# Performance work log

Measured on AMD Instinct MI355X. Metric: run time of the kernel, lower is better.

The kernel has to match this reference:

```python
import jax, jax.numpy as jnp
import numpy as np

N, B, T, D = 6, 4, 1024, 768
P = 3            # number of prior phases
H, Dh = 2, 32    # n_heads, head_dim
I = H * Dh       # inner_dim
EPS = 1e-5


def setup_inputs() -> dict:
    key = jax.random.key(0)
    ks = jax.random.split(key, 9)
    current_states = jax.random.normal(ks[0], (N, B, T, D), dtype=jnp.float32)
    history_states = jax.random.normal(ks[1], (P, N, B, T, D), dtype=jnp.float32)
    attention_mask = jax.random.randint(ks[2], (B, T), 0, 2, dtype=jnp.int32)
    # Linear weights stored as [in, out] (transposed nn.Linear weight)
    s = 1.0 / np.sqrt(D)
    Wq = jax.random.uniform(ks[3], (N, D, I), jnp.float32, -s, s)  # per-domain q proj
    Wk = jax.random.uniform(ks[4], (D, I), jnp.float32, -s, s)     # shared k proj
    Wv = jax.random.uniform(ks[5], (D, I), jnp.float32, -s, s)     # shared v proj
    so = 1.0 / np.sqrt(I)
    Wo = jax.random.uniform(ks[6], (N, I, D), jnp.float32, -so, so)  # per-domain out proj
    gamma = jnp.ones((N, D), jnp.float32)   # per-domain LayerNorm weight
    beta = jnp.zeros((N, D), jnp.float32)   # per-domain LayerNorm bias
    return {"current_states": current_states, "history_states": history_states,
            "attention_mask": attention_mask, "Wq": Wq, "Wk": Wk, "Wv": Wv,
            "Wo": Wo, "gamma": gamma, "beta": beta}


def reference(current_states, history_states, attention_mask, Wq, Wk, Wv, Wo, gamma, beta):
    x = current_states                                   # [N,B,T,D]
    # concat prior phases along time per domain: [N,B,P*T,D]
    prior = jnp.transpose(history_states, (1, 2, 0, 3, 4)).reshape(N, B, P * T, D)

    q = jnp.einsum('nbtd,ndi->nbti', x, Wq).reshape(N, B, T, H, Dh).transpose(0, 1, 3, 2, 4)       # [N,B,H,T,Dh]
    k = jnp.einsum('nbsd,di->nbsi', prior, Wk).reshape(N, B, P * T, H, Dh).transpose(0, 1, 3, 2, 4)  # [N,B,H,S,Dh]
    v = jnp.einsum('nbsd,di->nbsi', prior, Wv).reshape(N, B, P * T, H, Dh).transpose(0, 1, 3, 2, 4)

    scale = 1.0 / jnp.sqrt(jnp.float32(Dh))
    scores = jnp.einsum('nbhtd,nbhsd->nbhts', q, k) * scale  # [N,B,H,T,P*T]
    full_mask = jnp.tile(attention_mask.astype(jnp.float32), (1, P))  # [B,P*T]
    bias = (1.0 - full_mask)[None, :, None, None, :] * -10000.0
    attn = jax.nn.softmax(scores + bias, axis=-1)
    o = jnp.einsum('nbhts,nbhsd->nbhtd', attn, v)            # [N,B,H,T,Dh]
    o = o.transpose(0, 1, 3, 2, 4).reshape(N, B, T, I)       # [N,B,T,I]
    o = jnp.einsum('nbti,nid->nbtd', o, Wo)                  # [N,B,T,D]

    y = x + o  # residual (dropout p=0)
    mu = jnp.mean(y, axis=-1, keepdims=True)
    var = jnp.mean(jnp.square(y - mu), axis=-1, keepdims=True)
    out = (y - mu) * jax.lax.rsqrt(var + EPS)
    out = out * gamma[:, None, None, :] + beta[:, None, None, :]
    return out
```

## Files before the change

### kernel.cpp

```cpp
#include <hip/hip_runtime.h>
#include <hip/hip_bf16.h>
#include <math.h>

#define NDOM 6
#define BB 4
#define TT 1024
#define DD 768
#define PP 3
#define HH 2
#define DHH 32
#define II 64
#define SS (PP*TT)
#define NROW (NDOM*BB*TT)
#define NKVROW (NDOM*BB*SS)
#define NSPLIT 8
#define NITER (SS/NSPLIT/64)
#define NKVB (NKVROW/128)
#define NQB  (NROW/128)
#define LNEPS 1e-5f

typedef unsigned int uint;
typedef uint  u32x4  __attribute__((ext_vector_type(4)));
typedef int   i32x2  __attribute__((ext_vector_type(2)));
typedef float f32x2  __attribute__((ext_vector_type(2)));
typedef float f32x4  __attribute__((ext_vector_type(4)));
typedef float f32x16 __attribute__((ext_vector_type(16)));
typedef __bf16 bf16x8 __attribute__((ext_vector_type(8)));

__device__ __forceinline__ f32x16 mfma32(u32x4 a, u32x4 b, f32x16 c) {
  return __builtin_amdgcn_mfma_f32_32x32x16_bf16(
      __builtin_bit_cast(bf16x8, a), __builtin_bit_cast(bf16x8, b), c, 0, 0, 0);
}

__device__ __forceinline__ uint pkbf(float a, float b) {
  union { __bf16 h[2]; uint u; } v;
  v.h[0] = (__bf16)a; v.h[1] = (__bf16)b;
  return v.u;
}
__device__ __forceinline__ float b2f(uint u16) {
  union { uint i; float f; } v; v.i = u16 << 16; return v.f;
}

__device__ __forceinline__ void plswap(uint a, uint b, uint& x, uint& y) {
#if __has_builtin(__builtin_amdgcn_permlane32_swap)
  i32x2 r = __builtin_amdgcn_permlane32_swap((int)a, (int)b, false, false);
  x = (uint)r.x; y = (uint)r.y;
#else
  uint sa = __shfl_xor(a, 32), sb = __shfl_xor(b, 32);
  bool h1 = (threadIdx.x & 32) != 0;
  x = h1 ? sb : a;
  y = h1 ? b : sa;
#endif
}

#if __has_builtin(__builtin_amdgcn_global_load_lds)
#define HAS_GLL 1
typedef __attribute__((address_space(3))) uint lds_u32;
typedef __attribute__((address_space(1))) uint glb_u32;
__device__ __forceinline__ void gll16(const void* src, void* lds_base) {
  __builtin_amdgcn_global_load_lds((const glb_u32*)src, (lds_u32*)lds_base, 16, 0, 0);
}
#else
#define HAS_GLL 0
#endif

__global__ __launch_bounds__(256) void prep_kernel(
    const int* __restrict__ mask, const float* __restrict__ Wk,
    const float* __restrict__ Wv, const float* __restrict__ Wq,
    const float* __restrict__ Wo,
    __hip_bfloat16* __restrict__ Bkv, __hip_bfloat16* __restrict__ Bq,
    __hip_bfloat16* __restrict__ Bo, float* __restrict__ bias2)
{
  int i = blockIdx.x * 256 + threadIdx.x;
  const int N1 = 128 * 768;
  const int N2 = NDOM * 64 * 768;
  const int N3 = NDOM * 768 * 64;
  if (i < N1) {
    int c = i / 768, kd = i % 768;
    int e = kd & 7, ud = (kd >> 3) & 7, kk = kd >> 6;
    int k = (kk << 6) + ((ud ^ (c & 7)) << 3) + e;
    float v = (c < 64) ? Wk[k * 64 + c] : Wv[k * 64 + (c - 64)];
    Bkv[i] = __float2bfloat16(v);
  } else if (i < N1 + N2) {
    int j = i - N1;
    int n = j / (64 * 768);
    int rem = j % (64 * 768);
    int c = rem / 768, kd = rem % 768;
    int e = kd & 7, ud = (kd >> 3) & 7, kk = kd >> 6;
    int k = (kk << 6) + ((ud ^ (c & 7)) << 3) + e;
    Bq[j] = __float2bfloat16(Wq[((size_t)n * 768 + k) * 64 + c]);
  } else if (i < N1 + N2 + N3) {
    int j = i - N1 - N2;
    int n = j / (768 * 64);
    int rem = j % (768 * 64);
    int d = rem / 64, k = rem % 64;
    Bo[j] = __float2bfloat16(Wo[((size_t)n * 64 + k) * 768 + d]);
  } else if (i < N1 + N2 + N3 + BB * SS) {
    int j = i - N1 - N2 - N3;
    int b = j / SS, s = j % SS;
    bias2[j] = (1.0f - (float)mask[b * TT + (s & (TT - 1))]) * (-14426.950408889634f);
  }
}

__global__ __launch_bounds__(256) void qkv_gemm_kernel(
    const float* __restrict__ x, const float* __restrict__ hist,
    const __hip_bfloat16* __restrict__ Bkv, const __hip_bfloat16* __restrict__ Bq,
    __hip_bfloat16* __restrict__ Qo, __hip_bfloat16* __restrict__ Kh,
    __hip_bfloat16* __restrict__ Vt2)
{
  __shared__ float As[128 * 64];
  __shared__ __hip_bfloat16 Bs[128 * 64];
  const int tid = threadIdx.x;
  const int lane = tid & 63, w = tid >> 6;
  const int cl = lane & 31, hi = lane >> 5;

  const bool isKV = blockIdx.x < NKVB;
  const float* Asrc;
  int nb = 0, s0 = 0, n = 0, brow = 0;
  if (isKV) {
    brow = blockIdx.x * 128;
    nb = brow / SS; n = nb >> 2;
    int b = nb & 3;
    s0 = brow % SS;
    int p = s0 / TT, t0 = s0 % TT;
    Asrc = hist + (((size_t)(p * NDOM + n) * BB + b) * TT + t0) * 768;
  } else {
    brow = (blockIdx.x - NKVB) * 128;
    n = brow >> 12;
    Asrc = x + (size_t)brow * 768;
  }
  const __hip_bfloat16* Bsrc = isKV ? Bkv : (Bq + (size_t)n * 64 * 768);
  const int BROWS = isKV ? 128 : 64;
  const int NACC = isKV ? 4 : 2;

  f32x16 acc[4] = {};

  const int lrow16 = lane >> 4, lslot16 = lane & 15;
  const int lrow8  = lane >> 3, lslot8  = lane & 7;

  for (int kk = 0; kk < 12; ++kk) {
#pragma unroll
    for (int j = 0; j < 8; ++j) {
      int row0 = w * 32 + j * 4;
      int row = row0 + lrow16;
      int gs = lslot16 ^ (row & 15);
      const float* src = Asrc + (size_t)row * 768 + kk * 64 + gs * 4;
#if HAS_GLL
      gll16(src, &As[row0 * 64]);
#else
      *(f32x4*)(&As[row0 * 64] + lane * 4) = *(const f32x4*)src;
#endif
    }
    {
      int perw = BROWS / 4;
#pragma unroll
      for (int j = 0; j < 4; ++j) {
        if (j * 8 < perw) {
          int c0 = w * perw + j * 8;
          int c = c0 + lrow8;
          const __hip_bfloat16* src = Bsrc + (size_t)c * 768 + kk * 64 + lslot8 * 8;
#if HAS_GLL
          gll16(src, &Bs[c0 * 64]);
#else
          *(u32x4*)(&Bs[c0 * 64] + lane * 8) = *(const u32x4*)src;
#endif
        }
      }
    }
    __syncthreads();

    {
      const int row = w * 32 + cl;
#pragma unroll
      for (int ks = 0; ks < 4; ++ks) {
        int t = ks * 4 + hi * 2;
        f32x4 a0 = *(const f32x4*)&As[row * 64 + ((t       ^ (row & 15)) * 4)];
        f32x4 a1 = *(const f32x4*)&As[row * 64 + (((t + 1) ^ (row & 15)) * 4)];
        u32x4 a = {pkbf(a0.x, a0.y), pkbf(a0.z, a0.w), pkbf(a1.x, a1.y), pkbf(a1.z, a1.w)};
        int u0 = ks * 2 + hi;
#pragma unroll
        for (int g = 0; g < 4; ++g) {
          if (g < NACC) {
            int c = g * 32 + cl;
            u32x4 b = *(const u32x4*)&Bs[c * 64 + ((u0 ^ (c & 7)) * 8)];
            acc[g] = mfma32(a, b, acc[g]);
          }
        }
      }
    }
    __syncthreads();
  }

  if (isKV) {
    {
      const size_t base0 = (size_t)(nb * 2 + 0) * SS;
      const size_t base1 = (size_t)(nb * 2 + 1) * SS;
#pragma unroll
      for (int r = 0; r < 16; ++r) {
        int rl = (r & 3) + 8 * (r >> 2) + 4 * hi;
        int s  = s0 + w * 32 + rl;
        Kh[(base0 + s) * 32 + cl] = __float2bfloat16(acc[0][r]);
        Kh[(base1 + s) * 32 + cl] = __float2bfloat16(acc[1][r]);
      }
    }
#pragma unroll
    for (int k = 0; k < 4; ++k) {
      int sb = (s0 + w * 32 + 8 * k) >> 3;
      size_t A0 = (((size_t)(nb * 2 + 0) * (SS / 8) + sb) * 32 + cl) * 8 + 4 * hi;
      size_t A1 = (((size_t)(nb * 2 + 1) * (SS / 8) + sb) * 32 + cl) * 8 + 4 * hi;
      *(uint2*)(Vt2 + A0) = uint2{pkbf(acc[2][4*k], acc[2][4*k+1]), pkbf(acc[2][4*k+2], acc[2][4*k+3])};
      *(uint2*)(Vt2 + A1) = uint2{pkbf(acc[3][4*k], acc[3][4*k+1]), pkbf(acc[3][4*k+2], acc[3][4*k+3])};
    }
  } else {
#pragma unroll
    for (int r = 0; r < 16; ++r) {
      int rl = (r & 3) + 8 * (r >> 2) + 4 * hi;
      size_t rb = (size_t)(brow + w * 32 + rl) * 64;
      Qo[rb + cl]      = __float2bfloat16(acc[0][r]);
      Qo[rb + 32 + cl] = __float2bfloat16(acc[1][r]);
    }
  }
}

struct KV { u32x4 k0, k1, k2, k3, v0, v1, v2, v3; };

__global__ __launch_bounds__(256) void attn_kernel(
    const __hip_bfloat16* __restrict__ Q, const __hip_bfloat16* __restrict__ Kh,
    const __hip_bfloat16* __restrict__ Vt2, const float* __restrict__ bias2,
    __hip_bfloat16* __restrict__ Op, float* __restrict__ Mp, float* __restrict__ Lp)
{
  const int tid = threadIdx.x;
  const int lane = tid & 63, w = tid >> 6;
  const int cl = lane & 31, hi = lane >> 5;
  const int bid = blockIdx.x;
  const int g = bid % 48;
  const int rest = bid / 48;
  const int sp = rest >> 3;
  const int tq = rest & 7;
  const int qtile = tq * 4 + w;
  const int h = g & 1, nb = g >> 1;
  const int b = nb & 3;
  const int qrow = nb * TT + qtile * 32;
  const int sbase = sp * (SS / NSPLIT);

  const __hip_bfloat16* Qp = Q + (size_t)(qrow + cl) * 64 + h * 32 + hi * 8;
  u32x4 qf0 = *(const u32x4*)Qp;
  u32x4 qf1 = *(const u32x4*)(Qp + 16);

  const __hip_bfloat16* Kp = Kh + ((size_t)(nb * 2 + h) * SS + sbase) * 32;
  const __hip_bfloat16* Vp = Vt2 + (size_t)(nb * 2 + h) * SS * 32 + (size_t)sbase * 32;
  const float* Bp = bias2 + b * SS + sbase + hi * 4;

  const float scale2 = 0.17677669529663687f * 1.4426950408889634f;
  const f32x2 sc2 = {scale2, scale2};

  f32x16 ot = {};
  float m = -1e30f, lsum = 0.f;

  auto loadKV = [&](int it) {
    KV t;
    const __hip_bfloat16* kp = Kp + (size_t)it * 64 * 32;
    t.k0 = *(const u32x4*)(kp + cl * 32 + hi * 8);
    t.k1 = *(const u32x4*)(kp + cl * 32 + 16 + hi * 8);
    t.k2 = *(const u32x4*)(kp + 1024 + cl * 32 + hi * 8);
    t.k3 = *(const u32x4*)(kp + 1024 + cl * 32 + 16 + hi * 8);
    const __hip_bfloat16* vp = Vp + (size_t)it * 64 * 32;
    t.v0 = *(const u32x4*)(vp + ((0 * 2 + hi) * 32 + cl) * 8);
    t.v1 = *(const u32x4*)(vp + ((1 * 2 + hi) * 32 + cl) * 8);
    t.v2 = *(const u32x4*)(vp + ((2 * 2 + hi) * 32 + cl) * 8);
    t.v3 = *(const u32x4*)(vp + ((3 * 2 + hi) * 32 + cl) * 8);
    return t;
  };

  auto compute = [&](const KV& t, int it) {
    f32x16 pz0 = {}, pz1 = {};
    pz0 = mfma32(t.k0, qf0, pz0);
    pz0 = mfma32(t.k1, qf1, pz0);
    pz1 = mfma32(t.k2, qf0, pz1);
    pz1 = mfma32(t.k3, qf1, pz1);
    const float* bp = Bp + it * 64;
    f32x4 b4[8];
#pragma unroll
    for (int q = 0; q < 8; ++q) b4[q] = *(const f32x4*)(bp + 8 * q);
    f32x2 p2[16];
#pragma unroll
    for (int i = 0; i < 8; ++i) {
      f32x4 bq0 = b4[i >> 1];
      f32x4 bq1 = b4[4 + (i >> 1)];
      f32x2 bv0 = (i & 1) ? f32x2{bq0.z, bq0.w} : f32x2{bq0.x, bq0.y};
      f32x2 bv1 = (i & 1) ? f32x2{bq1.z, bq1.w} : f32x2{bq1.x, bq1.y};
      p2[i]     = f32x2{pz0[2*i], pz0[2*i+1]} * sc2 + bv0;
      p2[8 + i] = f32x2{pz1[2*i], pz1[2*i+1]} * sc2 + bv1;
    }
    f32x2 mx = p2[0];
#pragma unroll
    for (int i = 1; i < 16; ++i) {
      mx.x = fmaxf(mx.x, p2[i].x);
      mx.y = fmaxf(mx.y, p2[i].y);
    }
    float tm = fmaxf(mx.x, mx.y);
    tm = fmaxf(tm, __shfl_xor(tm, 32));
    if (!__all(tm - m <= 8.f)) {
      float mn = fmaxf(m, tm);
      float f = exp2f(m - mn);
#pragma unroll
      for (int i = 0; i < 16; ++i) ot[i] *= f;
      lsum *= f;
      m = mn;
    }
    const f32x2 m2 = {m, m};
    f32x2 s2 = {0.f, 0.f};
#pragma unroll
    for (int i = 0; i < 16; ++i) {
      f32x2 d = p2[i] - m2;
      f32x2 e = {exp2f(d.x), exp2f(d.y)};
      p2[i] = e;
      s2 += e;
    }
    float ts = s2.x + s2.y;
    ts += __shfl_xor(ts, 32);
    lsum += ts;
    uint cv[16];
#pragma unroll
    for (int i = 0; i < 16; ++i) cv[i] = pkbf(p2[i].x, p2[i].y);
    u32x4 pf0, pf1, pf2, pf3;
    {
      uint x0, y0, x1, y1;
      plswap(cv[0], cv[2],  x0, y0); plswap(cv[1], cv[3],  x1, y1);
      pf0 = u32x4{x0, x1, y0, y1};
      plswap(cv[4], cv[6],  x0, y0); plswap(cv[5], cv[7],  x1, y1);
      pf1 = u32x4{x0, x1, y0, y1};
      plswap(cv[8], cv[10], x0, y0); plswap(cv[9], cv[11], x1, y1);
      pf2 = u32x4{x0, x1, y0, y1};
      plswap(cv[12], cv[14], x0, y0); plswap(cv[13], cv[15], x1, y1);
      pf3 = u32x4{x0, x1, y0, y1};
    }
    ot = mfma32(t.v0, pf0, ot);
    ot = mfma32(t.v1, pf1, ot);
    ot = mfma32(t.v2, pf2, ot);
    ot = mfma32(t.v3, pf3, ot);
  };

  KV cur = loadKV(0);
#pragma unroll 1
  for (int it = 0; it < NITER; ++it) {
    KV nxt = loadKV(it + 1 < NITER ? it + 1 : NITER - 1);
    compute(cur, it);
    cur = nxt;
    __builtin_amdgcn_s_barrier();
  }

  __hip_bfloat16* op = Op + ((size_t)sp * NROW + qrow + cl) * 64 + h * 32 + 4 * hi;
#pragma unroll
  for (int k = 0; k < 4; ++k) {
    uint2 wv = {pkbf(ot[4*k], ot[4*k+1]), pkbf(ot[4*k+2], ot[4*k+3])};
    *(uint2*)(op + 8 * k) = wv;
  }
  if (lane < 32) {
    int mi = ((sp * 24 + nb) * 2 + h) * TT + qtile * 32 + cl;
    Mp[mi] = m;
    Lp[mi] = lsum;
  }
}

__global__ __launch_bounds__(256) void oproj_ln_kernel(
    const float* __restrict__ x, const __hip_bfloat16* __restrict__ Op,
    const float* __restrict__ Mp, const float* __restrict__ Lp,
    const __hip_bfloat16* __restrict__ Bo, const float* __restrict__ gamma,
    const float* __restrict__ beta, float* __restrict__ out)
{
  __shared__ float red[4][32][2];
  __shared__ float redf[32][2];
  const int tid = threadIdx.x;
  const int lane = tid & 63, w = tid >> 6;
  const int cl = lane & 31, hi = lane >> 5;
  const int row0 = blockIdx.x * 32;
  const int n = row0 >> 12;
  const int nb = row0 >> 10;
  const int trow = (row0 & 1023) + cl;
  const int MLS = 24 * 2 * TT;

  float wsp[2][NSPLIT];
#pragma unroll
  for (int h = 0; h < 2; ++h) {
    int mi = (nb * 2 + h) * TT + trow;
    float mv[NSPLIT], lv[NSPLIT];
#pragma unroll
    for (int sp = 0; sp < NSPLIT; ++sp) { mv[sp] = Mp[mi + sp * MLS]; lv[sp] = Lp[mi + sp * MLS]; }
    float ms = mv[0];
#pragma unroll
    for (int sp = 1; sp < NSPLIT; ++sp) ms = fmaxf(ms, mv[sp]);
    float den = 0.f;
#pragma unroll
    for (int sp = 0; sp < NSPLIT; ++sp) { wsp[h][sp] = exp2f(mv[sp] - ms); den = fmaf(lv[sp], wsp[h][sp], den); }
    float inv = 1.0f / den;
#pragma unroll
    for (int sp = 0; sp < NSPLIT; ++sp) wsp[h][sp] *= inv;
  }

  u32x4 af[4];
#pragma unroll
  for (int ks = 0; ks < 4; ++ks) {
    int h = ks >> 1;
    size_t off = (size_t)(row0 + cl) * 64 + ks * 16 + hi * 8;
    f32x2 s0 = {}, s1 = {}, s2 = {}, s3 = {};
#pragma unroll
    for (int sp = 0; sp < NSPLIT; ++sp) {
      u32x4 v = *(const u32x4*)(Op + (size_t)sp * NROW * 64 + off);
      float wv = wsp[h][sp];
      s0 += f32x2{b2f(v[0] & 0xffffu), b2f(v[0] >> 16)} * wv;
      s1 += f32x2{b2f(v[1] & 0xffffu), b2f(v[1] >> 16)} * wv;
      s2 += f32x2{b2f(v[2] & 0xffffu), b2f(v[2] >> 16)} * wv;
      s3 += f32x2{b2f(v[3] & 0xffffu), b2f(v[3] >> 16)} * wv;
    }
    af[ks] = u32x4{pkbf(s0.x, s0.y), pkbf(s1.x, s1.y), pkbf(s2.x, s2.y), pkbf(s3.x, s3.y)};
  }

  const __hip_bfloat16* Bp = Bo + ((size_t)n * 768 + w * 192 + cl) * 64 + hi * 8;
  f32x16 acc[6] = {};
#pragma unroll
  for (int ks = 0; ks < 4; ++ks) {
#pragma unroll
    for (int t = 0; t < 6; ++t) {
      u32x4 bb = *(const u32x4*)(Bp + (size_t)(t * 32) * 64 + ks * 16);
      acc[t] = mfma32(af[ks], bb, acc[t]);
    }
  }

  float s1[16], s2[16];
#pragma unroll
  for (int r = 0; r < 16; ++r) { s1[r] = 0.f; s2[r] = 0.f; }
#pragma unroll
  for (int t = 0; t < 6; ++t) {
#pragma unroll
    for (int r = 0; r < 16; ++r) {
      int R = (r & 3) + 8 * (r >> 2) + 4 * hi;
      int col = w * 192 + t * 32 + cl;
      float y = acc[t][r] + x[(size_t)(row0 + R) * 768 + col];
      acc[t][r] = y;
      s1[r] += y;
      s2[r] = fmaf(y, y, s2[r]);
    }
  }
#pragma unroll
  for (int r = 0; r < 16; ++r) {
#pragma unroll
    for (int off = 1; off < 32; off <<= 1) {
      s1[r] += __shfl_xor(s1[r], off);
      s2[r] += __shfl_xor(s2[r], off);
    }
  }
  if (cl == 0) {
#pragma unroll
    for (int r = 0; r < 16; ++r) {
      int R = (r & 3) + 8 * (r >> 2) + 4 * hi;
      red[w][R][0] = s1[r];
      red[w][R][1] = s2[r];
    }
  }
  __syncthreads();
  if (tid < 64) {
    int R = tid & 31, st = tid >> 5;
    redf[R][st] = red[0][R][st] + red[1][R][st] + red[2][R][st] + red[3][R][st];
  }
  __syncthreads();

  float gv[6], bv[6];
#pragma unroll
  for (int t = 0; t < 6; ++t) {
    int col = w * 192 + t * 32 + cl;
    gv[t] = gamma[n * 768 + col];
    bv[t] = beta[n * 768 + col];
  }
#pragma unroll
  for (int r = 0; r < 16; ++r) {
    int R = (r & 3) + 8 * (r >> 2) + 4 * hi;
    float mu = redf[R][0] * (1.0f / 768.0f);
    float var = redf[R][1] * (1.0f / 768.0f) - mu * mu;
    float rs = rsqrtf(var + LNEPS);
#pragma unroll
    for (int t = 0; t < 6; ++t) {
      int col = w * 192 + t * 32 + cl;
      out[(size_t)(row0 + R) * 768 + col] = (acc[t][r] - mu) * rs * gv[t] + bv[t];
    }
  }
}

extern "C" void kernel_launch(void* const* d_in, const int* in_sizes, int n_in,
                              void* d_out, int out_size, void* d_ws, size_t ws_size,
                              hipStream_t stream) {
  const float* x     = (const float*)d_in[0];
  const float* hist  = (const float*)d_in[1];
  const int*   mask  = (const int*)d_in[2];
  const float* Wq    = (const float*)d_in[3];
  const float* Wk    = (const float*)d_in[4];
  const float* Wv    = (const float*)d_in[5];
  const float* Wo    = (const float*)d_in[6];
  const float* gamma = (const float*)d_in[7];
  const float* beta  = (const float*)d_in[8];
  float* out = (float*)d_out;

  char* ws = (char*)d_ws;
  __hip_bfloat16* Qb  = (__hip_bfloat16*)ws;  ws += (size_t)NROW * II * 2;
  __hip_bfloat16* Kh  = (__hip_bfloat16*)ws;  ws += (size_t)NKVROW * II * 2;
  __hip_bfloat16* Vt2 = (__hip_bfloat16*)ws;  ws += (size_t)NKVROW * II * 2;
  __hip_bfloat16* Op  = (__hip_bfloat16*)ws;  ws += (size_t)NSPLIT * NROW * II * 2;
  float* Mp           = (float*)ws;           ws += (size_t)NSPLIT * 24 * 2 * TT * 4;
  float* Lp           = (float*)ws;           ws += (size_t)NSPLIT * 24 * 2 * TT * 4;
  __hip_bfloat16* Bkv = (__hip_bfloat16*)ws;  ws += (size_t)128 * 768 * 2;
  __hip_bfloat16* Bq  = (__hip_bfloat16*)ws;  ws += (size_t)NDOM * 64 * 768 * 2;
  __hip_bfloat16* Bo  = (__hip_bfloat16*)ws;  ws += (size_t)NDOM * 768 * 64 * 2;
  float* bias2        = (float*)ws;           ws += (size_t)BB * SS * 4;

  const int PREP_N = 128*768 + NDOM*64*768 + NDOM*768*64 + BB*SS;
  prep_kernel<<<(PREP_N + 255) / 256, 256, 0, stream>>>(mask, Wk, Wv, Wq, Wo, Bkv, Bq, Bo, bias2);
  qkv_gemm_kernel<<<NKVB + NQB, 256, 0, stream>>>(x, hist, Bkv, Bq, Qb, Kh, Vt2);
  attn_kernel<<<48 * 8 * NSPLIT, 256, 0, stream>>>(Qb, Kh, Vt2, bias2, Op, Mp, Lp);
  oproj_ln_kernel<<<NROW / 32, 256, 0, stream>>>(x, Op, Mp, Lp, Bo, gamma, beta, out);
}
```

Before: 210.2 us.

## Double-buffer QKV GEMM with 32-wide K slices and halve attention splits

The QKV projection GEMM now stages K-slices of 32 into two LDS buffers and prefetches the next slice while computing the current one. Explicit vmcnt waits and raw barriers replace the two __syncthreads per iteration, so the global-to-LDS latency can be hidden behind MFMA work. The weight swizzle in the prep kernel is changed to match the narrower XOR pattern. NSPLIT is also reduced from 8 to 4, which halves the number of KV splits in attention and gives each block more iterations, trading parallelism for fewer partial results to merge.

```diff
diff --git a/kernel.cpp b/kernel.cpp
--- a/kernel.cpp
+++ b/kernel.cpp
@@ -13,7 +13,7 @@
 #define SS (PP*TT)
 #define NROW (NDOM*BB*TT)
 #define NKVROW (NDOM*BB*SS)
-#define NSPLIT 8
+#define NSPLIT 4
 #define NITER (SS/NSPLIT/64)
 #define NKVB (NKVROW/128)
 #define NQB  (NROW/128)
@@ -77,8 +77,8 @@
   const int N3 = NDOM * 768 * 64;
   if (i < N1) {
     int c = i / 768, kd = i % 768;
-    int e = kd & 7, ud = (kd >> 3) & 7, kk = kd >> 6;
-    int k = (kk << 6) + ((ud ^ (c & 7)) << 3) + e;
+    int e = kd & 7, ud = (kd >> 3) & 3, kk = kd >> 5;
+    int k = (kk << 5) + ((ud ^ (c & 3)) << 3) + e;
     float v = (c < 64) ? Wk[k * 64 + c] : Wv[k * 64 + (c - 64)];
     Bkv[i] = __float2bfloat16(v);
   } else if (i < N1 + N2) {
@@ -86,8 +86,8 @@
     int n = j / (64 * 768);
     int rem = j % (64 * 768);
     int c = rem / 768, kd = rem % 768;
-    int e = kd & 7, ud = (kd >> 3) & 7, kk = kd >> 6;
-    int k = (kk << 6) + ((ud ^ (c & 7)) << 3) + e;
+    int e = kd & 7, ud = (kd >> 3) & 3, kk = kd >> 5;
+    int k = (kk << 5) + ((ud ^ (c & 3)) << 3) + e;
     Bq[j] = __float2bfloat16(Wq[((size_t)n * 768 + k) * 64 + c]);
   } else if (i < N1 + N2 + N3) {
     int j = i - N1 - N2;
@@ -108,8 +108,8 @@
     __hip_bfloat16* __restrict__ Qo, __hip_bfloat16* __restrict__ Kh,
     __hip_bfloat16* __restrict__ Vt2)
 {
-  __shared__ float As[128 * 64];
-  __shared__ __hip_bfloat16 Bs[128 * 64];
+  __shared__ float As[2][128 * 32];
+  __shared__ __hip_bfloat16 Bs[2][128 * 32];
   const int tid = threadIdx.x;
   const int lane = tid & 63, w = tid >> 6;
   const int cl = lane & 31, hi = lane >> 5;
@@ -130,68 +130,76 @@
     Asrc = x + (size_t)brow * 768;
   }
   const __hip_bfloat16* Bsrc = isKV ? Bkv : (Bq + (size_t)n * 64 * 768);
-  const int BROWS = isKV ? 128 : 64;
-  const int NACC = isKV ? 4 : 2;
+
+  const int lrowA = lane >> 3, lslotA = lane & 7;
+  const int lrowB = lane >> 2, lslotB = lane & 3;
+
+  auto stageA = [&](int h, int buf) {
+#pragma unroll
+    for (int j = 0; j < 4; ++j) {
+      int row0 = w * 32 + j * 8;
+      int row = row0 + lrowA;
+      int gs = lslotA ^ (row & 7);
+      const float* src = Asrc + (size_t)row * 768 + h * 32 + gs * 4;
+#if HAS_GLL
+      gll16(src, &As[buf][row0 * 32]);
+#else
+      *(f32x4*)(&As[buf][row0 * 32] + lane * 4) = *(const f32x4*)src;
+#endif
+    }
+  };
+  auto stageB = [&](int h, int buf, int nglB) {
+#pragma unroll
+    for (int j = 0; j < 2; ++j) {
+      if (j < nglB) {
+        int c0 = w * 16 * nglB + j * 16;
+        int c = c0 + lrowB;
+        const __hip_bfloat16* src = Bsrc + (size_t)c * 768 + h * 32 + lslotB * 8;
+#if HAS_GLL
+        gll16(src, &Bs[buf][c0 * 32]);
+#else
+        *(u32x4*)(&Bs[buf][c0 * 32] + lane * 8) = *(const u32x4*)src;
+#endif
+      }
+    }
+  };
 
   f32x16 acc[4] = {};
-
-  const int lrow16 = lane >> 4, lslot16 = lane & 15;
-  const int lrow8  = lane >> 3, lslot8  = lane & 7;
-
-  for (int kk = 0; kk < 12; ++kk) {
-#pragma unroll
-    for (int j = 0; j < 8; ++j) {
-      int row0 = w * 32 + j * 4;
-      int row = row0 + lrow16;
-      int gs = lslot16 ^ (row & 15);
-      const float* src = Asrc + (size_t)row * 768 + kk * 64 + gs * 4;
-#if HAS_GLL
-      gll16(src, &As[row0 * 64]);
-#else
-      *(f32x4*)(&As[row0 * 64] + lane * 4) = *(const f32x4*)src;
-#endif
-    }
-    {
-      int perw = BROWS / 4;
-#pragma unroll
-      for (int j = 0; j < 4; ++j) {
-        if (j * 8 < perw) {
-          int c0 = w * perw + j * 8;
-          int c = c0 + lrow8;
-          const __hip_bfloat16* src = Bsrc + (size_t)c * 768 + kk * 64 + lslot8 * 8;
-#if HAS_GLL
-          gll16(src, &Bs[c0 * 64]);
-#else
-          *(u32x4*)(&Bs[c0 * 64] + lane * 8) = *(const u32x4*)src;
-#endif
+  const int rowR = w * 32 + cl;
+
+  auto computeHalf = [&](int buf, int NACC) {
+#pragma unroll
+    for (int ks = 0; ks < 2; ++ks) {
+      int t = ks * 4 + hi * 2;
+      f32x4 a0 = *(const f32x4*)&As[buf][rowR * 32 + ((t       ^ (rowR & 7)) * 4)];
+      f32x4 a1 = *(const f32x4*)&As[buf][rowR * 32 + (((t + 1) ^ (rowR & 7)) * 4)];
+      u32x4 a = {pkbf(a0.x, a0.y), pkbf(a0.z, a0.w), pkbf(a1.x, a1.y), pkbf(a1.z, a1.w)};
+      int u0 = ks * 2 + hi;
+#pragma unroll
+      for (int g = 0; g < 4; ++g) {
+        if (g < NACC) {
+          int c = g * 32 + cl;
+          u32x4 b = *(const u32x4*)&Bs[buf][c * 32 + ((u0 ^ (c & 3)) * 8)];
+          acc[g] = mfma32(a, b, acc[g]);
         }
       }
     }
-    __syncthreads();
-
-    {
-      const int row = w * 32 + cl;
-#pragma unroll
-      for (int ks = 0; ks < 4; ++ks) {
-        int t = ks * 4 + hi * 2;
-        f32x4 a0 = *(const f32x4*)&As[row * 64 + ((t       ^ (row & 15)) * 4)];
-        f32x4 a1 = *(const f32x4*)&As[row * 64 + (((t + 1) ^ (row & 15)) * 4)];
-        u32x4 a = {pkbf(a0.x, a0.y), pkbf(a0.z, a0.w), pkbf(a1.x, a1.y), pkbf(a1.z, a1.w)};
-        int u0 = ks * 2 + hi;
-#pragma unroll
-        for (int g = 0; g < 4; ++g) {
-          if (g < NACC) {
-            int c = g * 32 + cl;
-            u32x4 b = *(const u32x4*)&Bs[c * 64 + ((u0 ^ (c & 7)) * 8)];
-            acc[g] = mfma32(a, b, acc[g]);
-          }
-        }
+  };
+
+  if (isKV) {
+    stageA(0, 0); stageB(0, 0, 2);
+#pragma unroll 2
+    for (int h = 0; h < 24; ++h) {
+      if (h + 1 < 24) {
+        stageA(h + 1, (h + 1) & 1); stageB(h + 1, (h + 1) & 1, 2);
+        asm volatile("s_waitcnt vmcnt(6)" ::: "memory");
+      } else {
+        asm volatile("s_waitcnt vmcnt(0)" ::: "memory");
       }
-    }
-    __syncthreads();
-  }
-
-  if (isKV) {
+      __builtin_amdgcn_s_barrier();
+      computeHalf(h & 1, 4);
+      __builtin_amdgcn_s_barrier();
+    }
     {
       const size_t base0 = (size_t)(nb * 2 + 0) * SS;
       const size_t base1 = (size_t)(nb * 2 + 1) * SS;
@@ -212,6 +220,19 @@
       *(uint2*)(Vt2 + A1) = uint2{pkbf(acc[3][4*k], acc[3][4*k+1]), pkbf(acc[3][4*k+2], acc[3][4*k+3])};
     }
   } else {
+    stageA(0, 0); stageB(0, 0, 1);
+#pragma unroll 2
+    for (int h = 0; h < 24; ++h) {
+      if (h + 1 < 24) {
+        stageA(h + 1, (h + 1) & 1); stageB(h + 1, (h + 1) & 1, 1);
+        asm volatile("s_waitcnt vmcnt(5)" ::: "memory");
+      } else {
+        asm volatile("s_waitcnt vmcnt(0)" ::: "memory");
+      }
+      __builtin_amdgcn_s_barrier();
+      computeHalf(h & 1, 2);
+      __builtin_amdgcn_s_barrier();
+    }
 #pragma unroll
     for (int r = 0; r < 16; ++r) {
       int rl = (r & 3) + 8 * (r >> 2) + 4 * hi;
```

Measured after the change: 204.7 us. -2.6%, faster.
